# Kernel tuning notes

Hardware: AMD Instinct MI355X
Metric: run time of the kernel (lower is better)

## Reference

```python
import jax, jax.numpy as jnp
import numpy as np

TAU = 2.0  # LIF membrane time constant (spikingjelly default)
SCALE = 0.125

@jax.custom_vjp
def heaviside(x):
    return (x >= 0).astype(x.dtype)

def _hv_fwd(x):
    return heaviside(x), x

def _hv_bwd(x, g):
    s = jax.nn.sigmoid(4.0 * x)  # sigmoid surrogate, alpha=4
    return (g * 4.0 * s * (1.0 - s),)

heaviside.defvjp(_hv_fwd, _hv_bwd)

def lif(x, v_th):
    """Multi-step LIF over leading time axis. x: [T, ...]. decay_input, hard reset to 0."""
    def step(v, xt):
        v = v + (xt - v) / TAU
        s = heaviside(v - v_th)
        return v * (1.0 - s), s
    return jax.lax.scan(step, jnp.zeros_like(x[0]), x)[1]

def conv1x1(x, w, b=None):
    # x: [T,B,C,N], w: [O,C]
    y = jnp.einsum('oc,tbcn->tbon', w, x)
    if b is not None:
        y = y + b[None, None, :, None]
    return y

def bn(x, p, eps=1e-5):
    # inference-mode BatchNorm1d over channel axis; p: [4,C] = gamma,beta,mean,var
    g, b, m, v = p[0], p[1], p[2], p[3]
    inv = g / jnp.sqrt(v + eps)
    return x * inv[None, None, :, None] + (b - m * inv)[None, None, :, None]

def setup_inputs() -> dict:
    key = jax.random.key(0)
    ks = jax.random.split(key, 10)
    T, B, C, H, W = 4, 32, 512, 16, 16
    wscale = 1.0 / np.sqrt(C)
    def bn_params(k):
        k1, k2, k3, k4 = jax.random.split(k, 4)
        gamma = 1.0 + 0.1 * jax.random.normal(k1, (C,))
        beta = 0.1 * jax.random.normal(k2, (C,))
        mean = 0.1 * jax.random.normal(k3, (C,))
        var = 1.0 + 0.1 * jax.random.uniform(k4, (C,))
        return jnp.stack([gamma, beta, mean, var])
    return {
        'x': jax.random.normal(ks[0], (T, B, C, H, W), dtype=jnp.float32),
        'res_attn': jnp.zeros((1,), dtype=jnp.float32),
        'q_w': wscale * jax.random.normal(ks[1], (C, C), dtype=jnp.float32),
        'k_w': wscale * jax.random.normal(ks[2], (C, C), dtype=jnp.float32),
        'v_w': wscale * jax.random.normal(ks[3], (C, C), dtype=jnp.float32),
        'proj_w': wscale * jax.random.normal(ks[4], (C, C), dtype=jnp.float32),
        'proj_b': 0.01 * jax.random.normal(ks[5], (C,), dtype=jnp.float32),
        'q_bn': bn_params(ks[6]),
        'k_bn': bn_params(ks[7]),
        'v_bn': bn_params(ks[8]),
        'p_bn': bn_params(ks[9]),
    }

def reference(x, res_attn, q_w, k_w, v_w, proj_w, proj_b, q_bn, k_bn, v_bn, p_bn):
    T, B, C, H, W = x.shape
    num_heads = 8
    d = C // num_heads
    N = H * W
    xf = x.reshape(T, B, C, N)

    def branch(w, p, v_th):
        return lif(bn(conv1x1(xf, w), p), v_th)

    def to_heads(t):  # [T,B,C,N] -> [T,B,h,N,d]
        return t.transpose(0, 1, 3, 2).reshape(T, B, N, num_heads, d).transpose(0, 1, 3, 2, 4)

    q = to_heads(branch(q_w, q_bn, 1.0))
    k = to_heads(branch(k_w, k_bn, 1.0))
    v = to_heads(branch(v_w, v_bn, 1.0))

    # linear (non-softmax) attention: q @ (k^T @ v) * scale
    kv = jnp.einsum('tbhnd,tbhne->tbhde', k, v)
    a = jnp.einsum('tbhnd,tbhde->tbhne', q, kv) * SCALE  # [T,B,h,N,d]

    # [T,B,h,N,d] -> transpose(3,4) -> [T,B,h,d,N] -> [T,B,C,N]
    a = jnp.swapaxes(a, 3, 4).reshape(T, B, C, N)
    a = lif(a, 0.5)  # attn_lif with v_threshold=0.5

    out = conv1x1(a, proj_w, proj_b)
    out = bn(out, p_bn).reshape(T, B, C, H, W)
    out = lif(out, 1.0)
    return out, v
```

## Files before the change

kernel.cpp:

```cpp
#include <hip/hip_runtime.h>
#include <stdint.h>

#define T_ 4
#define B_ 32
#define C_ 512
#define N_ 256
#define NH_ 8
#define NB_ (N_ / 8)
#define BITS_BYTES_ ((size_t)(T_ * B_ * C_) * NB_)

typedef float f32x2 __attribute__((ext_vector_type(2)));

__device__ __forceinline__ f32x2 pk_mul_d(f32x2 a, f32x2 b) {
  f32x2 r;
  asm("v_pk_mul_f32 %0, %1, %2" : "=v"(r) : "v"(a), "v"(b));
  return r;
}
__device__ __forceinline__ f32x2 pk_mul_x(f32x2 a, f32x2 b) {
  f32x2 r;
  asm("v_pk_mul_f32 %0, %1, %2 op_sel:[0,1] op_sel_hi:[1,0]"
      : "=v"(r) : "v"(a), "v"(b));
  return r;
}
__device__ __forceinline__ void pk_add_acc(f32x2& acc, f32x2 p) {
  asm("v_pk_add_f32 %0, %0, %1" : "+v"(acc) : "v"(p));
}
__device__ __forceinline__ void pk_fma_d(f32x2& acc, f32x2 a, f32x2 b) {
  asm("v_pk_fma_f32 %0, %1, %2, %0" : "+v"(acc) : "v"(a), "v"(b));
}
__device__ __forceinline__ void pk_fma_x(f32x2& acc, f32x2 a, f32x2 b) {
  asm("v_pk_fma_f32 %0, %1, %2, %0 op_sel:[0,1,0] op_sel_hi:[1,0,1]"
      : "+v"(acc) : "v"(a), "v"(b));
}


__global__ __launch_bounds__(256, 2) void qkv_gemm_lif(
    const float* __restrict__ x, const float* __restrict__ wq,
    const float* __restrict__ wk, const float* __restrict__ wv,
    const float* __restrict__ bnq, const float* __restrict__ bnk,
    const float* __restrict__ bnv,
    uint8_t* __restrict__ sbits, float* __restrict__ out1) {
#pragma clang fp contract(off)
  const int bx = blockIdx.x;
  const int br = bx >> 4;
  const int tile = bx & 15;
  const int b  = blockIdx.y;
  const int ot = tile >> 1, nt = tile & 1;
  const float* w = (br == 0) ? wq : (br == 1) ? wk : wv;
  const float* bn = (br == 0) ? bnq : (br == 1) ? bnk : bnv;
  uint8_t* sb = sbits + (size_t)br * BITS_BYTES_;

  const int tid = threadIdx.x;
  const int tx = tid & 15, ty = tid >> 4;
  const int o0 = ot * 64, n0 = nt * 128;

  __shared__ float As[16][64];
  __shared__ float Bs[16][128];

  float inv[4], add[4];
#pragma unroll
  for (int i = 0; i < 4; ++i) {
    int o = o0 + ty * 4 + i;
    float g = bn[o], be = bn[C_ + o], mm = bn[2 * C_ + o], va = bn[3 * C_ + o];
    float iv = g / sqrtf(va + 1e-5f);
    inv[i] = iv;
    add[i] = be - mm * iv;
  }

  float vst[4][8];
#pragma unroll
  for (int i = 0; i < 4; ++i)
#pragma unroll
    for (int j = 0; j < 8; ++j) vst[i][j] = 0.f;

  for (int t = 0; t < T_; ++t) {
    const float* xb = x + (size_t)(t * B_ + b) * (C_ * N_);
    f32x2 acc_d[2][4], acc_x[2][4];
#pragma unroll
    for (int ip = 0; ip < 2; ++ip)
#pragma unroll
      for (int jp = 0; jp < 4; ++jp) {
        acc_d[ip][jp] = (f32x2){0.f, 0.f};
        acc_x[ip][jp] = (f32x2){0.f, 0.f};
      }

    for (int kc = 0; kc < C_; kc += 16) {
      int o = tid & 63, kq = (tid >> 6) * 4;
      float4 a4 = *(const float4*)(w + (size_t)(o0 + o) * C_ + kc + kq);
      int fr = tid >> 5, fq = (tid & 31) * 4;
      int fr2 = (tid + 256) >> 5, fq2 = ((tid + 256) & 31) * 4;
      float4 b40 = *(const float4*)(xb + (size_t)(kc + fr) * N_ + n0 + fq);
      float4 b41 = *(const float4*)(xb + (size_t)(kc + fr2) * N_ + n0 + fq2);
      __syncthreads();
      As[kq + 0][o] = a4.x; As[kq + 1][o] = a4.y;
      As[kq + 2][o] = a4.z; As[kq + 3][o] = a4.w;
      *(float4*)(&Bs[fr][fq]) = b40;
      *(float4*)(&Bs[fr2][fq2]) = b41;
      __syncthreads();
#pragma unroll
      for (int k = 0; k < 16; ++k) {
        float4 av4 = *(const float4*)(&As[k][ty * 4]);
        float4 bq0 = *(const float4*)(&Bs[k][tx * 4]);
        float4 bq1 = *(const float4*)(&Bs[k][64 + tx * 4]);
        f32x2 a2[2] = {(f32x2){av4.x, av4.y}, (f32x2){av4.z, av4.w}};
        f32x2 b2[4] = {(f32x2){bq0.x, bq0.y}, (f32x2){bq0.z, bq0.w},
                       (f32x2){bq1.x, bq1.y}, (f32x2){bq1.z, bq1.w}};
#pragma unroll
        for (int ip = 0; ip < 2; ++ip)
#pragma unroll
          for (int jp = 0; jp < 4; ++jp) {
            f32x2 pd = pk_mul_d(a2[ip], b2[jp]);
            f32x2 px = pk_mul_x(a2[ip], b2[jp]);
            pk_add_acc(acc_d[ip][jp], pd);
            pk_add_acc(acc_x[ip][jp], px);
          }
      }
    }
    __syncthreads();

    {
      size_t tb = (size_t)(t * B_ + b);
      unsigned nibsA = 0, nibsB = 0;
#pragma unroll
      for (int i = 0; i < 4; ++i) {
#pragma unroll
        for (int jj = 0; jj < 8; ++jj) {
          int ip = i >> 1, il = i & 1, jp = jj >> 1, jl = jj & 1;
          float a = (il == jl) ? acc_d[ip][jp][il] : acc_x[ip][jp][il];
          float y0 = a * inv[i];
          float y = y0 + add[i];
          float d = y - vst[i][jj];
          float vs = vst[i][jj] + d * 0.5f;
          unsigned sp = (vs >= 1.0f) ? 1u : 0u;
          vst[i][jj] = sp ? 0.f : vs;
          if (jj < 4) nibsA |= sp << (4 * i + jj);
          else        nibsB |= sp << (4 * i + jj - 4);
        }
      }
      unsigned oA = __shfl_xor(nibsA, 1);
      unsigned oB = __shfl_xor(nibsB, 1);
      int m = tx >> 1;
      if ((tx & 1) == 0) {
#pragma unroll
        for (int i = 0; i < 4; ++i) {
          int o = o0 + ty * 4 + i;
          unsigned byte_ = ((nibsA >> (4 * i)) & 0xF) | (((oA >> (4 * i)) & 0xF) << 4);
          sb[(tb * C_ + o) * NB_ + (n0 >> 3) + m] = (uint8_t)byte_;
        }
      } else {
#pragma unroll
        for (int i = 0; i < 4; ++i) {
          int o = o0 + ty * 4 + i;
          unsigned byte_ = ((oB >> (4 * i)) & 0xF) | (((nibsB >> (4 * i)) & 0xF) << 4);
          sb[(tb * C_ + o) * NB_ + (n0 >> 3) + 8 + m] = (uint8_t)byte_;
        }
      }
      if (br == 2) {
#pragma unroll
        for (int i = 0; i < 4; ++i) {
          int o = o0 + ty * 4 + i;
          int h = o >> 6, dd = o & 63;
          size_t base = ((tb * NH_ + h) * (size_t)N_) * 64 + dd;
#pragma unroll
          for (int jj = 0; jj < 8; ++jj) {
            int n = n0 + ((jj < 4) ? (tx * 4 + jj) : (64 + tx * 4 + jj - 4));
            unsigned sp = (jj < 4) ? ((nibsA >> (4 * i + jj)) & 1u)
                                   : ((nibsB >> (4 * i + jj - 4)) & 1u);
            out1[base + (size_t)n * 64] = sp ? 1.0f : 0.0f;
          }
        }
      }
    }
  }
}

__global__ __launch_bounds__(512, 1) void attn_lif(
    const uint8_t* __restrict__ bits, uint8_t* __restrict__ abits) {
#pragma clang fp contract(off)
  const unsigned long long* qb = (const unsigned long long*)bits;
  const unsigned long long* kb = qb + BITS_BYTES_ / 8;
  const unsigned long long* vb = kb + BITS_BYTES_ / 8;
  unsigned long long* ap = (unsigned long long*)abits;

  const int h = blockIdx.x, b = blockIdx.y;
  const int tid = threadIdx.x;
  const int lane = tid & 63, wave = tid >> 6;
  const int nw = wave & 3, eh = wave >> 2;

  __shared__ unsigned long long kbl[64][4];
  __shared__ unsigned long long vbl[64][4];
  __shared__ float kvl[64][64];

  float state[32];
#pragma unroll
  for (int e = 0; e < 32; ++e) state[e] = 0.f;

  for (int t = 0; t < T_; ++t) {
    size_t row0 = (size_t)(t * B_ + b) * C_ + h * 64;
    {
      int i = tid & 255, c = i >> 2, w = i & 3;
      if (tid < 256) kbl[c][w] = kb[(row0 + c) * 4 + w];
      else           vbl[c][w] = vb[(row0 + c) * 4 + w];
    }
    __syncthreads();
    {
      int d = tid & 63, eb = (tid >> 6) * 8;
#pragma unroll
      for (int e2 = 0; e2 < 8; ++e2) {
        int e = eb + e2;
        int s = 0;
#pragma unroll
        for (int w = 0; w < 4; ++w) s += __popcll(kbl[d][w] & vbl[e][w]);
        kvl[d][e] = (float)s;
      }
    }
    __syncthreads();
    float acc[32];
#pragma unroll
    for (int e = 0; e < 32; ++e) acc[e] = 0.f;
    for (int d = 0; d < 64; ++d) {
      unsigned long long qw = qb[(row0 + d) * 4 + nw];
      float qf = (float)(unsigned)((qw >> lane) & 1ULL);
      const float* kr = &kvl[d][eh * 32];
#pragma unroll
      for (int e = 0; e < 32; ++e) acc[e] = acc[e] + qf * kr[e];
    }
    {
#pragma unroll
      for (int e2 = 0; e2 < 32; ++e2) {
        int e = eh * 32 + e2;
        float a = acc[e2] * 0.125f;
        float d0 = a - state[e2];
        float vs = state[e2] + d0 * 0.5f;
        int sp = (vs >= 0.5f) ? 1 : 0;
        state[e2] = sp ? 0.f : vs;
        unsigned long long m = __ballot(sp);
        if (lane == 0) ap[(row0 + e) * 4 + nw] = m;
      }
    }
    __syncthreads();
  }
}

__global__ __launch_bounds__(256, 2) void proj_gemm_lif(
    const uint8_t* __restrict__ ab, const float* __restrict__ wp,
    const float* __restrict__ pb, const float* __restrict__ bnp,
    float* __restrict__ out0) {
  const int b = blockIdx.y;
  const int ot = blockIdx.x >> 1, nt = blockIdx.x & 1;
  const int tid = threadIdx.x;
  const int tx = tid & 15, ty = tid >> 4;
  const int o0 = ot * 64, n0 = nt * 128;

  __shared__ float As[2][16][64];
  __shared__ float Bs[2][16][128];

  float inv[4], add[4], bias[4];
  {
#pragma clang fp contract(off)
#pragma unroll
    for (int i = 0; i < 4; ++i) {
      int o = o0 + ty * 4 + i;
      float g = bnp[o], be = bnp[C_ + o], mm = bnp[2 * C_ + o], va = bnp[3 * C_ + o];
      float iv = g / sqrtf(va + 1e-5f);
      inv[i] = iv;
      add[i] = be - mm * iv;
      bias[i] = pb[o];
    }
  }

  float vst[4][8];
#pragma unroll
  for (int i = 0; i < 4; ++i)
#pragma unroll
    for (int j = 0; j < 8; ++j) vst[i][j] = 0.f;

  const int sa_o = tid & 63, sa_kq = (tid >> 6) * 4;
  const int br_ = tid >> 4, bq16 = tid & 15;

  for (int t = 0; t < T_; ++t) {
    f32x2 acc_d[2][4], acc_x[2][4];
#pragma unroll
    for (int ip = 0; ip < 2; ++ip)
#pragma unroll
      for (int jp = 0; jp < 4; ++jp) {
        acc_d[ip][jp] = (f32x2){0.f, 0.f};
        acc_x[ip][jp] = (f32x2){0.f, 0.f};
      }
    size_t tb = (size_t)(t * B_ + b);

    {
      float4 a4 = *(const float4*)(wp + (size_t)(o0 + sa_o) * C_ + 0 + sa_kq);
      uint8_t by = ab[(tb * C_ + 0 + br_) * NB_ + (n0 >> 3) + bq16];
      __syncthreads();
      As[0][sa_kq + 0][sa_o] = a4.x; As[0][sa_kq + 1][sa_o] = a4.y;
      As[0][sa_kq + 2][sa_o] = a4.z; As[0][sa_kq + 3][sa_o] = a4.w;
      int nb = bq16 * 8;
#pragma unroll
      for (int j = 0; j < 8; ++j) Bs[0][br_][nb + j] = (float)((by >> j) & 1);
      __syncthreads();
    }

    for (int it = 0; it < 32; ++it) {
      const int cur = it & 1;
      float4 a4; uint8_t by = 0;
      if (it < 31) {
        int kc = (it + 1) * 16;
        a4 = *(const float4*)(wp + (size_t)(o0 + sa_o) * C_ + kc + sa_kq);
        by = ab[(tb * C_ + kc + br_) * NB_ + (n0 >> 3) + bq16];
      }
#pragma unroll
      for (int k = 0; k < 16; ++k) {
        float4 av4 = *(const float4*)(&As[cur][k][ty * 4]);
        float4 bq0 = *(const float4*)(&Bs[cur][k][tx * 4]);
        float4 bq1 = *(const float4*)(&Bs[cur][k][64 + tx * 4]);
        f32x2 a2[2] = {(f32x2){av4.x, av4.y}, (f32x2){av4.z, av4.w}};
        f32x2 b2[4] = {(f32x2){bq0.x, bq0.y}, (f32x2){bq0.z, bq0.w},
                       (f32x2){bq1.x, bq1.y}, (f32x2){bq1.z, bq1.w}};
#pragma unroll
        for (int ip = 0; ip < 2; ++ip)
#pragma unroll
          for (int jp = 0; jp < 4; ++jp) {
            pk_fma_d(acc_d[ip][jp], a2[ip], b2[jp]);
            pk_fma_x(acc_x[ip][jp], a2[ip], b2[jp]);
          }
      }
      if (it < 31) {
        const int nxt = cur ^ 1;
        As[nxt][sa_kq + 0][sa_o] = a4.x; As[nxt][sa_kq + 1][sa_o] = a4.y;
        As[nxt][sa_kq + 2][sa_o] = a4.z; As[nxt][sa_kq + 3][sa_o] = a4.w;
        int nb = bq16 * 8;
#pragma unroll
        for (int j = 0; j < 8; ++j) Bs[nxt][br_][nb + j] = (float)((by >> j) & 1);
        __syncthreads();
      }
    }

    {
#pragma clang fp contract(off)
#pragma unroll
      for (int i = 0; i < 4; ++i) {
        int o = o0 + ty * 4 + i;
        float4 r0, r1;
#pragma unroll
        for (int jj = 0; jj < 8; ++jj) {
          int ip = i >> 1, il = i & 1, jp = jj >> 1, jl = jj & 1;
          float a = (il == jl) ? acc_d[ip][jp][il] : acc_x[ip][jp][il];
          float y1 = a + bias[i];
          float y2 = y1 * inv[i];
          float y = y2 + add[i];
          float d0 = y - vst[i][jj];
          float vs = vst[i][jj] + d0 * 0.5f;
          int sp = (vs >= 1.0f) ? 1 : 0;
          vst[i][jj] = sp ? 0.f : vs;
          if (jj < 4) (&r0.x)[jj] = sp ? 1.0f : 0.0f;
          else        (&r1.x)[jj - 4] = sp ? 1.0f : 0.0f;
        }
        float* dst = out0 + (tb * C_ + o) * N_ + n0;
        *(float4*)(dst + tx * 4) = r0;
        *(float4*)(dst + 64 + tx * 4) = r1;
      }
    }
  }
}


extern "C" void kernel_launch(void* const* d_in, const int* in_sizes, int n_in,
                              void* d_out, int out_size, void* d_ws, size_t ws_size,
                              hipStream_t stream) {
  const float* x   = (const float*)d_in[0];
  const float* qw  = (const float*)d_in[2];
  const float* kw  = (const float*)d_in[3];
  const float* vw  = (const float*)d_in[4];
  const float* pw  = (const float*)d_in[5];
  const float* pbb = (const float*)d_in[6];
  const float* qbn = (const float*)d_in[7];
  const float* kbn = (const float*)d_in[8];
  const float* vbn = (const float*)d_in[9];
  const float* pbn = (const float*)d_in[10];

  uint8_t* bits  = (uint8_t*)d_ws;
  uint8_t* abits = bits + 3 * BITS_BYTES_;

  float* out0 = (float*)d_out;
  float* out1 = out0 + (size_t)T_ * B_ * C_ * N_;

  qkv_gemm_lif<<<dim3(48, 32), dim3(256), 0, stream>>>(
      x, qw, kw, vw, qbn, kbn, vbn, bits, out1);
  attn_lif<<<dim3(8, 32), dim3(512), 0, stream>>>(bits, abits);
  proj_gemm_lif<<<dim3(16, 32), dim3(256), 0, stream>>>(abits, pw, pbb, pbn,
                                                        out0);
}
```

Before: 1.263 ms.

## Load x tile straight into LDS with global_load_lds and double the K tile

The x (B operand) tile of the QKV GEMM is now fetched with global_load_lds 16-byte direct-to-LDS loads instead of going through VGPRs and ds_write. The K step per iteration grows from 16 to 32, and the weight loads are widened to two float4 per thread. This halves the number of barrier pairs per GEMM and cuts register pressure and LDS store instructions. The cost is twice the LDS per block and a reliance on correct vmcnt waiting before the barrier. A redundant trailing barrier after the K loop is also dropped.

```diff
diff --git a/kernel.cpp b/kernel.cpp
--- a/kernel.cpp
+++ b/kernel.cpp
@@ -31,6 +31,12 @@
 __device__ __forceinline__ void pk_fma_x(f32x2& acc, f32x2 a, f32x2 b) {
   asm("v_pk_fma_f32 %0, %1, %2, %0 op_sel:[0,1,0] op_sel_hi:[1,0,1]"
       : "+v"(acc) : "v"(a), "v"(b));
+}
+
+__device__ __forceinline__ void gload_lds16(const void* g, void* l) {
+  __builtin_amdgcn_global_load_lds(
+      (const __attribute__((address_space(1))) unsigned int*)g,
+      (__attribute__((address_space(3))) unsigned int*)l, 16, 0, 0);
 }
 
 
@@ -54,8 +60,8 @@
   const int tx = tid & 15, ty = tid >> 4;
   const int o0 = ot * 64, n0 = nt * 128;
 
-  __shared__ float As[16][64];
-  __shared__ float Bs[16][128];
+  __shared__ float As[32][64];
+  __shared__ float Bs[32][128];
 
   float inv[4], add[4];
 #pragma unroll
@@ -73,6 +79,9 @@
 #pragma unroll
     for (int j = 0; j < 8; ++j) vst[i][j] = 0.f;
 
+  const int sa_o = tid & 63, sa_k8 = (tid >> 6) * 8;
+  const int wv_ = tid >> 6;
+
   for (int t = 0; t < T_; ++t) {
     const float* xb = x + (size_t)(t * B_ + b) * (C_ * N_);
     f32x2 acc_d[2][4], acc_x[2][4];
@@ -84,21 +93,26 @@
         acc_x[ip][jp] = (f32x2){0.f, 0.f};
       }
 
-    for (int kc = 0; kc < C_; kc += 16) {
-      int o = tid & 63, kq = (tid >> 6) * 4;
-      float4 a4 = *(const float4*)(w + (size_t)(o0 + o) * C_ + kc + kq);
-      int fr = tid >> 5, fq = (tid & 31) * 4;
-      int fr2 = (tid + 256) >> 5, fq2 = ((tid + 256) & 31) * 4;
-      float4 b40 = *(const float4*)(xb + (size_t)(kc + fr) * N_ + n0 + fq);
-      float4 b41 = *(const float4*)(xb + (size_t)(kc + fr2) * N_ + n0 + fq2);
+    for (int kc = 0; kc < C_; kc += 32) {
+      const float* wrow = w + (size_t)(o0 + sa_o) * C_ + kc + sa_k8;
+      float4 a0 = *(const float4*)(wrow);
+      float4 a1 = *(const float4*)(wrow + 4);
       __syncthreads();
-      As[kq + 0][o] = a4.x; As[kq + 1][o] = a4.y;
-      As[kq + 2][o] = a4.z; As[kq + 3][o] = a4.w;
-      *(float4*)(&Bs[fr][fq]) = b40;
-      *(float4*)(&Bs[fr2][fq2]) = b41;
+#pragma unroll
+      for (int r = 0; r < 4; ++r) {
+        int slot0 = r * 256 + wv_ * 64;
+        int slot = slot0 + (tid & 63);
+        int row = slot >> 5, col = (slot & 31) * 4;
+        gload_lds16(xb + (size_t)(kc + row) * N_ + n0 + col,
+                    (char*)&Bs[0][0] + (size_t)slot0 * 16);
+      }
+      As[sa_k8 + 0][sa_o] = a0.x; As[sa_k8 + 1][sa_o] = a0.y;
+      As[sa_k8 + 2][sa_o] = a0.z; As[sa_k8 + 3][sa_o] = a0.w;
+      As[sa_k8 + 4][sa_o] = a1.x; As[sa_k8 + 5][sa_o] = a1.y;
+      As[sa_k8 + 6][sa_o] = a1.z; As[sa_k8 + 7][sa_o] = a1.w;
       __syncthreads();
 #pragma unroll
-      for (int k = 0; k < 16; ++k) {
+      for (int k = 0; k < 32; ++k) {
         float4 av4 = *(const float4*)(&As[k][ty * 4]);
         float4 bq0 = *(const float4*)(&Bs[k][tx * 4]);
         float4 bq1 = *(const float4*)(&Bs[k][64 + tx * 4]);
@@ -116,7 +130,6 @@
           }
       }
     }
-    __syncthreads();
 
     {
       size_t tb = (size_t)(t * B_ + b);
```

Measured after the change: 1.240 ms. About the same (-1.8%).
